# Kernel optimization log

Measured on AMD Instinct MI355X. Metric: run time of the kernel, lower is better.

The kernel has to match this reference:

```python
import jax, jax.numpy as jnp
import numpy as np

N_HEADS = 16
EPS = 1e-12  # torch F.normalize eps


def setup_inputs() -> dict:
    key = jax.random.key(0)
    ks = jax.random.split(key, 10)
    bs, qlen, dim = 2, 2048, 1024
    s = 1.0 / np.sqrt(dim)
    inp = {
        "x": jax.random.normal(ks[0], (bs, qlen, dim), dtype=jnp.float32),
        "mask": jnp.ones((bs, qlen), dtype=jnp.int32),
        "Wq": jax.random.normal(ks[1], (dim, dim), dtype=jnp.float32) * s,
        "bq": jnp.zeros((dim,), dtype=jnp.float32),
        "Wk": jax.random.normal(ks[2], (dim, dim), dtype=jnp.float32) * s,
        "bk": jnp.zeros((dim,), dtype=jnp.float32),
        "Wv": jax.random.normal(ks[3], (dim, dim), dtype=jnp.float32) * s,
        "bv": jnp.zeros((dim,), dtype=jnp.float32),
        "Wo": jax.random.normal(ks[4], (dim, dim), dtype=jnp.float32) * s,
        "bo": jnp.zeros((dim,), dtype=jnp.float32),
        "scale": jnp.asarray(1.0 / np.sqrt(dim // N_HEADS), dtype=jnp.float32),
    }
    return inp


def reference(x, mask, Wq, bq, Wk, bk, Wv, bv, Wo, bo, scale):
    bs, qlen, dim = x.shape
    dph = dim // N_HEADS

    def shape_heads(t):  # [b, s, dim] -> [b, h, s, dph]
        return t.reshape(bs, -1, N_HEADS, dph).transpose(0, 2, 1, 3)

    q = shape_heads(x @ Wq + bq)
    k = shape_heads(x @ Wk + bk)
    v = shape_heads(x @ Wv + bv)

    # cosine attention: L2-normalize q, k; learned scalar scale
    q = q / jnp.maximum(jnp.linalg.norm(q, axis=-1, keepdims=True), EPS)
    k = k / jnp.maximum(jnp.linalg.norm(k, axis=-1, keepdims=True), EPS)
    q = q * scale

    scores = jnp.einsum("bhqd,bhkd->bhqk", q, k)  # [b,h,q,k]
    pad = (mask == 0)[:, None, None, :]  # [b,1,1,k]
    scores = jnp.where(pad, -jnp.inf, scores)
    weights = jax.nn.softmax(scores.astype(jnp.float32), axis=-1).astype(scores.dtype)
    ctx = jnp.einsum("bhqk,bhkd->bhqd", weights, v)
    ctx = ctx.transpose(0, 2, 1, 3).reshape(bs, qlen, dim)
    return ctx @ Wo + bo
```

## Files before the change

kernel.cpp:

```cpp
#include <hip/hip_runtime.h>
#include <math.h>

#define SEQ 2048
#define DIM 1024
#define NH 16
#define DPH 64
#define MTOT 4096

typedef __attribute__((ext_vector_type(8))) short bf16x8;
typedef __attribute__((ext_vector_type(4))) float f32x4;
typedef __attribute__((ext_vector_type(16))) float f32x16;
typedef __attribute__((ext_vector_type(4))) unsigned int u32x4;

__device__ __forceinline__ unsigned short f2bf(float f) {
    unsigned int u = __float_as_uint(f);
    return (unsigned short)((u + 0x7FFFu + ((u >> 16) & 1u)) >> 16);
}
__device__ __forceinline__ float bf2f(unsigned short h) {
    return __uint_as_float(((unsigned int)h) << 16);
}

__device__ __forceinline__ void stage16(const void* g, void* lds) {
    __builtin_amdgcn_global_load_lds((const __attribute__((address_space(1))) void*)g,
                                     (__attribute__((address_space(3))) void*)lds,
                                     16, 0, 0);
}

__device__ __forceinline__ unsigned cvtpk(float lo, float hi) {
    unsigned w;
    asm("v_cvt_pk_bf16_f32 %0, %1, %2" : "=v"(w) : "v"(lo), "v"(hi));
    return w;
}
__device__ __forceinline__ void plswap(unsigned &a, unsigned &b) {
    asm("v_permlane32_swap_b32 %0, %1" : "+v"(a), "+v"(b));
}

__device__ __forceinline__ void xcd_remap(int gx, int gy, int gz,
                                          int &x, int &y, int &z)
{
    const int h = (blockIdx.z * gy + blockIdx.y) * gx + blockIdx.x;
    const int nb = gx * gy * gz;
    const int chunk = nb >> 3;
    const int l = (h & 7) * chunk + (h >> 3);
    const int P = gx * gz;
    y = l / P;
    const int r = l - y * P;
    z = r / gx;
    x = r - z * gx;
}

__global__ __launch_bounds__(256) void cast_x(const float* __restrict__ X,
                                              unsigned short* __restrict__ Xb)
{
    size_t i = (size_t)blockIdx.x * 256 + threadIdx.x;
    float4 v = *(const float4*)&X[i * 4];
    ushort4 o;
    o.x = f2bf(v.x); o.y = f2bf(v.y); o.z = f2bf(v.z); o.w = f2bf(v.w);
    *(ushort4*)&Xb[i * 4] = o;
}

__global__ __launch_bounds__(256) void prep_w(
    const float* __restrict__ Wq, const float* __restrict__ Wk,
    const float* __restrict__ Wv, const float* __restrict__ Wo,
    unsigned short* __restrict__ Wqt, unsigned short* __restrict__ Wkt,
    unsigned short* __restrict__ Wvt, unsigned short* __restrict__ Wot)
{
    const float* W; unsigned short* Wt;
    switch (blockIdx.z) {
        case 0: W = Wq; Wt = Wqt; break;
        case 1: W = Wk; Wt = Wkt; break;
        case 2: W = Wv; Wt = Wvt; break;
        default: W = Wo; Wt = Wot; break;
    }
    __shared__ float T[32][33];
    const int t = threadIdx.x;
    const int kt0 = blockIdx.y * 32;
    const int nt0 = blockIdx.x * 32;
    const int r = t >> 3, c4 = (t & 7) * 4;
    float4 v = *(const float4*)&W[(size_t)(kt0 + r) * DIM + nt0 + c4];
    T[r][c4 + 0] = v.x; T[r][c4 + 1] = v.y; T[r][c4 + 2] = v.z; T[r][c4 + 3] = v.w;
    __syncthreads();
    ushort4 o;
    o.x = f2bf(T[c4 + 0][r]);
    o.y = f2bf(T[c4 + 1][r]);
    o.z = f2bf(T[c4 + 2][r]);
    o.w = f2bf(T[c4 + 3][r]);
    *(ushort4*)&Wt[(size_t)(nt0 + r) * DIM + kt0 + c4] = o;
}

__global__ __launch_bounds__(256) void pack_mask(const int* __restrict__ mask,
                                                 unsigned long long* __restrict__ MB)
{
    const int w = blockIdx.x * 4 + (threadIdx.x >> 6);
    const int lane = threadIdx.x & 63;
    const int b = w >> 5, kt = w & 31;
    int m = mask[b * SEQ + kt * 64 + lane];
    unsigned long long bits = __ballot(m != 0);
    if (lane == 0) MB[w] = bits;
}

__device__ __forceinline__ void gemm_core(
    const unsigned short* __restrict__ Ab, const unsigned short* __restrict__ Bt,
    const float* __restrict__ bias, unsigned short* __restrict__ Cb,
    float* __restrict__ Cf, int mode, int bx, int by, float qs)
{
    __shared__ __align__(16) unsigned short As[2][4096];
    __shared__ __align__(16) unsigned short Bs[2][4096];

    const int tid = threadIdx.x;
    const int l = tid & 63;
    const int w = tid >> 6;
    const int wm = w >> 1, wn = w & 1;
    const int lr = l & 15, lg = l >> 4;
    const int bm = by * 128;
    const int bn = bx * 128;

    const unsigned short* a_src0 = Ab + (size_t)(bm + (2 * w) * 16 + lr) * DIM + lg * 8;
    const unsigned short* a_src1 = Ab + (size_t)(bm + (2 * w + 1) * 16 + lr) * DIM + lg * 8;
    const unsigned short* b_src0 = Bt + (size_t)(bn + (2 * w) * 16 + lr) * DIM + lg * 8;
    const unsigned short* b_src1 = Bt + (size_t)(bn + (2 * w + 1) * 16 + lr) * DIM + lg * 8;

    f32x4 acc[4][4];
#pragma unroll
    for (int i = 0; i < 4; ++i)
#pragma unroll
        for (int j = 0; j < 4; ++j) acc[i][j] = (f32x4){0.f, 0.f, 0.f, 0.f};

    stage16(a_src0, &As[0][(2 * w) * 512]);
    stage16(a_src1, &As[0][(2 * w + 1) * 512]);
    stage16(b_src0, &Bs[0][(2 * w) * 512]);
    stage16(b_src1, &Bs[0][(2 * w + 1) * 512]);

    int t = 0;
    for (int kk = 0; kk < DIM; kk += 32) {
        __syncthreads();
        if (kk + 32 < DIM) {
            const int nxt = t ^ 1;
            stage16(a_src0 + kk + 32, &As[nxt][(2 * w) * 512]);
            stage16(a_src1 + kk + 32, &As[nxt][(2 * w + 1) * 512]);
            stage16(b_src0 + kk + 32, &Bs[nxt][(2 * w) * 512]);
            stage16(b_src1 + kk + 32, &Bs[nxt][(2 * w + 1) * 512]);
        }
        bf16x8 aF[4], bF[4];
#pragma unroll
        for (int i = 0; i < 4; ++i) {
            aF[i] = *(const bf16x8*)&As[t][(wm * 4 + i) * 512 + l * 8];
            bF[i] = *(const bf16x8*)&Bs[t][(wn * 4 + i) * 512 + l * 8];
        }
#pragma unroll
        for (int i = 0; i < 4; ++i)
#pragma unroll
            for (int j = 0; j < 4; ++j)
                acc[i][j] = __builtin_amdgcn_mfma_f32_16x16x32_bf16(aF[i], bF[j], acc[i][j], 0, 0, 0);
        t ^= 1;
    }

    float bvj[4];
#pragma unroll
    for (int j = 0; j < 4; ++j) bvj[j] = bias[bn + wn * 64 + j * 16 + lr];
#pragma unroll
    for (int i = 0; i < 4; ++i)
#pragma unroll
        for (int j = 0; j < 4; ++j)
#pragma unroll
            for (int p = 0; p < 4; ++p) acc[i][j][p] += bvj[j];

    if (mode == 0) {
#pragma unroll
        for (int i = 0; i < 4; ++i) {
            float scl[4];
#pragma unroll
            for (int p = 0; p < 4; ++p) {
                float s = 0.f;
#pragma unroll
                for (int j = 0; j < 4; ++j) s = fmaf(acc[i][j][p], acc[i][j][p], s);
                s += __shfl_xor(s, 1);
                s += __shfl_xor(s, 2);
                s += __shfl_xor(s, 4);
                s += __shfl_xor(s, 8);
                scl[p] = qs / fmaxf(sqrtf(s), 1e-12f);
            }
            const int m0 = bm + wm * 64 + i * 16 + lg * 4;
#pragma unroll
            for (int j = 0; j < 4; ++j) {
                const int n = bn + wn * 64 + j * 16 + lr;
#pragma unroll
                for (int p = 0; p < 4; ++p)
                    Cb[(size_t)(m0 + p) * DIM + n] = f2bf(acc[i][j][p] * scl[p]);
            }
        }
    } else if (mode == 1) {
#pragma unroll
        for (int i = 0; i < 4; ++i) {
            const int m0 = bm + wm * 64 + i * 16 + lg * 4;
            const int b = m0 >> 11, s = m0 & 2047;
#pragma unroll
            for (int j = 0; j < 4; ++j) {
                const int n = bn + wn * 64 + j * 16 + lr;
                const int h = n >> 6, d = n & 63;
                ushort4 o;
                o.x = f2bf(acc[i][j][0]);
                o.y = f2bf(acc[i][j][1]);
                o.z = f2bf(acc[i][j][2]);
                o.w = f2bf(acc[i][j][3]);
                *(ushort4*)&Cb[((size_t)((b * NH + h) * DPH + d)) * SEQ + s] = o;
            }
        }
    } else {
#pragma unroll
        for (int i = 0; i < 4; ++i) {
            const int m0 = bm + wm * 64 + i * 16 + lg * 4;
#pragma unroll
            for (int j = 0; j < 4; ++j) {
                const int n = bn + wn * 64 + j * 16 + lr;
#pragma unroll
                for (int p = 0; p < 4; ++p)
                    Cf[(size_t)(m0 + p) * DIM + n] = acc[i][j][p];
            }
        }
    }
}

__global__ __launch_bounds__(256) void qkv_gemm(
    const unsigned short* __restrict__ Xb,
    const unsigned short* __restrict__ Wqt, const unsigned short* __restrict__ Wkt,
    const unsigned short* __restrict__ Wvt,
    const float* __restrict__ bq, const float* __restrict__ bk, const float* __restrict__ bv,
    const float* __restrict__ scale_p,
    unsigned short* __restrict__ Qb, unsigned short* __restrict__ Kb,
    unsigned short* __restrict__ Vtb)
{
    int x, y, z;
    xcd_remap(8, 32, 3, x, y, z);
    if (z == 0)
        gemm_core(Xb, Wqt, bq, Qb, nullptr, 0, x, y, scale_p[0] * 1.44269504088896340736f);
    else if (z == 1)
        gemm_core(Xb, Wkt, bk, Kb, nullptr, 0, x, y, 1.0f);
    else
        gemm_core(Xb, Wvt, bv, Vtb, nullptr, 1, x, y, 1.0f);
}

__global__ __launch_bounds__(256) void o_gemm(
    const unsigned short* __restrict__ Ab, const unsigned short* __restrict__ Wot,
    const float* __restrict__ bo, float* __restrict__ Out)
{
    int x, y, z;
    xcd_remap(8, 32, 1, x, y, z);
    gemm_core(Ab, Wot, bo, nullptr, Out, 2, x, y, 1.0f);
}

__global__ __launch_bounds__(256) void attn(
    const unsigned short* __restrict__ Qb, const unsigned short* __restrict__ Kb,
    const unsigned short* __restrict__ Vtb, const unsigned long long* __restrict__ MB,
    unsigned short* __restrict__ CTXb)
{
    __shared__ __align__(16) unsigned short Ks[2][4096];
    __shared__ __align__(16) unsigned short Vts[2][4096];

    const int tid = threadIdx.x;
    const int l = tid & 63;
    const int w = tid >> 6;
    const int l31 = l & 31;
    const int hi = l >> 5;

    int qt, h, b;
    {
        const int hh = (blockIdx.z * 16 + blockIdx.y) * 16 + blockIdx.x;
        const int ll = (hh & 7) * 64 + (hh >> 3);
        qt = ll & 15;
        const int g = ll >> 4;
        h = g & 15;
        b = g >> 4;
    }

    const size_t qrow = (size_t)(b * SEQ + qt * 128 + w * 32 + l31);
    bf16x8 qf[4];
#pragma unroll
    for (int df = 0; df < 4; ++df)
        qf[df] = *(const bf16x8*)&Qb[qrow * DIM + h * DPH + df * 16 + hi * 8];

    const int sub = l >> 3, ss = (l & 7) ^ sub;
    const unsigned short* Kptr  = Kb  + (size_t)(b * SEQ) * DIM + h * DPH;
    const unsigned short* Vtptr = Vtb + ((size_t)(b * NH + h) * DPH) * SEQ;
    const unsigned long long* mbp = MB + b * 32;

    f32x16 ctx0 = {}, ctx1 = {};
    float lsum = 0.f;

    {
        const int r0 = w * 16, r1 = w * 16 + 8;
        stage16(Kptr + (size_t)(r0 + sub) * DIM + ss * 8, &Ks[0][r0 * 64]);
        stage16(Kptr + (size_t)(r1 + sub) * DIM + ss * 8, &Ks[0][r1 * 64]);
        stage16(Vtptr + (size_t)(r0 + sub) * SEQ + ss * 8, &Vts[0][r0 * 64]);
        stage16(Vtptr + (size_t)(r1 + sub) * SEQ + ss * 8, &Vts[0][r1 * 64]);
    }

    for (int kt = 0; kt < SEQ / 64; ++kt) {
        __syncthreads();
        const int cur = kt & 1;
        if (kt + 1 < SEQ / 64) {
            const int nxt = cur ^ 1;
            const int r0 = w * 16, r1 = w * 16 + 8;
            const size_t ko = (size_t)((kt + 1) * 64);
            stage16(Kptr + (ko + r0 + sub) * DIM + ss * 8, &Ks[nxt][r0 * 64]);
            stage16(Kptr + (ko + r1 + sub) * DIM + ss * 8, &Ks[nxt][r1 * 64]);
            stage16(Vtptr + (size_t)(r0 + sub) * SEQ + ko + ss * 8, &Vts[nxt][r0 * 64]);
            stage16(Vtptr + (size_t)(r1 + sub) * SEQ + ko + ss * 8, &Vts[nxt][r1 * 64]);
        }

        const char* kbase = (const char*)Ks[cur];
        f32x16 S0 = {}, S1 = {};
#pragma unroll
        for (int df = 0; df < 4; ++df) {
            const int so = ((df * 2 + hi) ^ (l31 & 7)) << 4;
            bf16x8 k0 = *(const bf16x8*)(kbase + l31 * 128 + so);
            bf16x8 k1 = *(const bf16x8*)(kbase + (32 + l31) * 128 + so);
            S0 = __builtin_amdgcn_mfma_f32_32x32x16_bf16(k0, qf[df], S0, 0, 0, 0);
            S1 = __builtin_amdgcn_mfma_f32_32x32x16_bf16(k1, qf[df], S1, 0, 0, 0);
        }

        float p[32];
#pragma unroll
        for (int r = 0; r < 16; ++r) {
            p[r]      = __builtin_amdgcn_exp2f(S0[r]);
            p[16 + r] = __builtin_amdgcn_exp2f(S1[r]);
        }

        const unsigned long long bits = mbp[kt];
        if (bits != ~0ull) {
#pragma unroll
            for (int r = 0; r < 16; ++r) {
                const int key0 = (r & 3) + 8 * (r >> 2) + 4 * hi;
                p[r]      *= (float)((bits >> key0) & 1);
                p[16 + r] *= (float)((bits >> (32 + key0)) & 1);
            }
        }

#pragma unroll
        for (int r = 0; r < 32; ++r) lsum += p[r];

        bf16x8 pa[4];
#pragma unroll
        for (int krow = 0; krow < 2; ++krow) {
            const float* pp = &p[krow * 16];
            unsigned w01[4], w23[4];
#pragma unroll
            for (int a = 0; a < 4; ++a) {
                w01[a] = cvtpk(pp[4 * a + 0], pp[4 * a + 1]);
                w23[a] = cvtpk(pp[4 * a + 2], pp[4 * a + 3]);
            }
#pragma unroll
            for (int fh = 0; fh < 2; ++fh) {
                unsigned A0 = w01[2 * fh], B0 = w01[2 * fh + 1];
                unsigned A1 = w23[2 * fh], B1 = w23[2 * fh + 1];
                plswap(A0, B0);
                plswap(A1, B1);
                u32x4 tt = {A0, A1, B0, B1};
                union { u32x4 u; bf16x8 v; } cvt;
                cvt.u = tt;
                pa[krow * 2 + fh] = cvt.v;
            }
        }

        const char* vbase = (const char*)Vts[cur];
#pragma unroll
        for (int kf2 = 0; kf2 < 4; ++kf2) {
            const int so = ((kf2 * 2 + hi) ^ (l31 & 7)) << 4;
            bf16x8 v0 = *(const bf16x8*)(vbase + l31 * 128 + so);
            bf16x8 v1 = *(const bf16x8*)(vbase + (32 + l31) * 128 + so);
            ctx0 = __builtin_amdgcn_mfma_f32_32x32x16_bf16(pa[kf2], v0, ctx0, 0, 0, 0);
            ctx1 = __builtin_amdgcn_mfma_f32_32x32x16_bf16(pa[kf2], v1, ctx1, 0, 0, 0);
        }
    }

    lsum += __shfl_xor(lsum, 32);
    const float inv = 1.0f / lsum;

    const size_t orow0 = (size_t)(b * SEQ + qt * 128 + w * 32);
#pragma unroll
    for (int r = 0; r < 16; ++r) {
        const int q = (r & 3) + 8 * (r >> 2) + 4 * hi;
        const float invr = __shfl(inv, q);
        const size_t ro = (orow0 + q) * DIM + h * DPH;
        CTXb[ro + l31]      = f2bf(ctx0[r] * invr);
        CTXb[ro + 32 + l31] = f2bf(ctx1[r] * invr);
    }
}

extern "C" void kernel_launch(void* const* d_in, const int* in_sizes, int n_in,
                              void* d_out, int out_size, void* d_ws, size_t ws_size,
                              hipStream_t stream)
{
    const float* x    = (const float*)d_in[0];
    const int*   mask = (const int*)d_in[1];
    const float* Wq   = (const float*)d_in[2];
    const float* bq   = (const float*)d_in[3];
    const float* Wk   = (const float*)d_in[4];
    const float* bk   = (const float*)d_in[5];
    const float* Wv   = (const float*)d_in[6];
    const float* bv   = (const float*)d_in[7];
    const float* Wo   = (const float*)d_in[8];
    const float* bo   = (const float*)d_in[9];
    const float* scale = (const float*)d_in[10];
    float* out = (float*)d_out;

    char* p = (char*)d_ws;
    unsigned short* Xb  = (unsigned short*)p; p += (size_t)MTOT * DIM * 2;
    unsigned short* Wqt = (unsigned short*)p; p += (size_t)DIM * DIM * 2;
    unsigned short* Wkt = (unsigned short*)p; p += (size_t)DIM * DIM * 2;
    unsigned short* Wvt = (unsigned short*)p; p += (size_t)DIM * DIM * 2;
    unsigned short* Wot = (unsigned short*)p; p += (size_t)DIM * DIM * 2;
    unsigned short* Qb  = (unsigned short*)p; p += (size_t)MTOT * DIM * 2;
    unsigned short* Kb  = (unsigned short*)p; p += (size_t)MTOT * DIM * 2;
    unsigned short* Vtb = (unsigned short*)p; p += (size_t)MTOT * DIM * 2;
    unsigned short* CTXb = (unsigned short*)p; p += (size_t)MTOT * DIM * 2;
    unsigned long long* MBits = (unsigned long long*)p;

    cast_x<<<dim3(MTOT * DIM / 4 / 256), 256, 0, stream>>>(x, Xb);
    prep_w<<<dim3(32, 32, 4), 256, 0, stream>>>(Wq, Wk, Wv, Wo, Wqt, Wkt, Wvt, Wot);
    pack_mask<<<dim3(16), 256, 0, stream>>>(mask, MBits);
    qkv_gemm<<<dim3(8, 32, 3), 256, 0, stream>>>(
        Xb, Wqt, Wkt, Wvt, bq, bk, bv, scale, Qb, Kb, Vtb);
    attn<<<dim3(16, 16, 2), 256, 0, stream>>>(Qb, Kb, Vtb, MBits, CTXb);
    o_gemm<<<dim3(8, 32, 1), 256, 0, stream>>>(CTXb, Wot, bo, out);
}
```

Before: 239.6 us.

## Triple-buffer GEMM LDS staging with partial vmcnt waits instead of full sync

Changes the projection GEMM main loop from double buffering to a three-stage LDS ring. Loads run two k-steps ahead, and each step waits only on the older batch of global-to-LDS loads (vmcnt(4)) before the barrier, rather than a __syncthreads that drains everything. The goal is to keep more memory latency in flight behind the MFMA work. In exchange, LDS use per block rises from 32KB to 48KB, which may lower occupancy, and the hand-written waitcnt accounting relies on the compiler issuing no other outstanding vector memory ops.

Result: slower. 249.7 us (+4.2%).

```diff
diff --git a/kernel.cpp b/kernel.cpp
--- a/kernel.cpp
+++ b/kernel.cpp
@@ -104,8 +104,8 @@
     const float* __restrict__ bias, unsigned short* __restrict__ Cb,
     float* __restrict__ Cf, int mode, int bx, int by, float qs)
 {
-    __shared__ __align__(16) unsigned short As[2][4096];
-    __shared__ __align__(16) unsigned short Bs[2][4096];
+    __shared__ __align__(16) unsigned short As[3 * 4096];
+    __shared__ __align__(16) unsigned short Bs[3 * 4096];
 
     const int tid = threadIdx.x;
     const int l = tid & 63;
@@ -120,39 +120,54 @@
     const unsigned short* b_src0 = Bt + (size_t)(bn + (2 * w) * 16 + lr) * DIM + lg * 8;
     const unsigned short* b_src1 = Bt + (size_t)(bn + (2 * w + 1) * 16 + lr) * DIM + lg * 8;
 
+    const int s0 = (2 * w) * 512, s1 = (2 * w + 1) * 512;
+
     f32x4 acc[4][4];
 #pragma unroll
     for (int i = 0; i < 4; ++i)
 #pragma unroll
         for (int j = 0; j < 4; ++j) acc[i][j] = (f32x4){0.f, 0.f, 0.f, 0.f};
 
-    stage16(a_src0, &As[0][(2 * w) * 512]);
-    stage16(a_src1, &As[0][(2 * w + 1) * 512]);
-    stage16(b_src0, &Bs[0][(2 * w) * 512]);
-    stage16(b_src1, &Bs[0][(2 * w + 1) * 512]);
-
-    int t = 0;
-    for (int kk = 0; kk < DIM; kk += 32) {
-        __syncthreads();
-        if (kk + 32 < DIM) {
-            const int nxt = t ^ 1;
-            stage16(a_src0 + kk + 32, &As[nxt][(2 * w) * 512]);
-            stage16(a_src1 + kk + 32, &As[nxt][(2 * w + 1) * 512]);
-            stage16(b_src0 + kk + 32, &Bs[nxt][(2 * w) * 512]);
-            stage16(b_src1 + kk + 32, &Bs[nxt][(2 * w + 1) * 512]);
-        }
+    stage16(a_src0, &As[s0]);
+    stage16(a_src1, &As[s1]);
+    stage16(b_src0, &Bs[s0]);
+    stage16(b_src1, &Bs[s1]);
+    stage16(a_src0 + 32, &As[4096 + s0]);
+    stage16(a_src1 + 32, &As[4096 + s1]);
+    stage16(b_src0 + 32, &Bs[4096 + s0]);
+    stage16(b_src1 + 32, &Bs[4096 + s1]);
+
+    int cur = 0;
+    int nx2 = 2;
+    for (int t = 0; t < 32; ++t) {
+        if (t == 31) asm volatile("s_waitcnt vmcnt(0)" ::: "memory");
+        else         asm volatile("s_waitcnt vmcnt(4)" ::: "memory");
+        __builtin_amdgcn_s_barrier();
+
+        if (t + 2 < 32) {
+            const int kk = (t + 2) * 32;
+            stage16(a_src0 + kk, &As[nx2 * 4096 + s0]);
+            stage16(a_src1 + kk, &As[nx2 * 4096 + s1]);
+            stage16(b_src0 + kk, &Bs[nx2 * 4096 + s0]);
+            stage16(b_src1 + kk, &Bs[nx2 * 4096 + s1]);
+        }
+
+        const unsigned short* Ap = &As[cur * 4096];
+        const unsigned short* Bp = &Bs[cur * 4096];
         bf16x8 aF[4], bF[4];
 #pragma unroll
         for (int i = 0; i < 4; ++i) {
-            aF[i] = *(const bf16x8*)&As[t][(wm * 4 + i) * 512 + l * 8];
-            bF[i] = *(const bf16x8*)&Bs[t][(wn * 4 + i) * 512 + l * 8];
+            aF[i] = *(const bf16x8*)&Ap[(wm * 4 + i) * 512 + l * 8];
+            bF[i] = *(const bf16x8*)&Bp[(wn * 4 + i) * 512 + l * 8];
         }
 #pragma unroll
         for (int i = 0; i < 4; ++i)
 #pragma unroll
             for (int j = 0; j < 4; ++j)
                 acc[i][j] = __builtin_amdgcn_mfma_f32_16x16x32_bf16(aF[i], bF[j], acc[i][j], 0, 0, 0);
-        t ^= 1;
+
+        cur = (cur == 2) ? 0 : cur + 1;
+        nx2 = (nx2 == 2) ? 0 : nx2 + 1;
     }
 
     float bvj[4];
```
